# Kernel optimization log

Hardware: AMD Instinct MI355X
Metric: run time of the kernel (lower is better)

The kernel has to match this reference:

```python
import jax, jax.numpy as jnp
import numpy as np

SHIFT_CONSTRAINT = 1000.0
TWO_PI = 2.0 * np.pi


def setup_inputs() -> dict:
    key = jax.random.key(0)
    k1, k2, k3, k4 = jax.random.split(key, 4)
    N, M, rank = 1000, 4000, 8
    X = jax.random.normal(k1, (N, M), dtype=jnp.float32)
    C_tilde = jax.random.uniform(k2, (rank, N), dtype=jnp.float32)
    S_tilde = jax.random.uniform(k3, (N, rank), dtype=jnp.float32)
    tau_tilde = jax.random.normal(k4, (N, rank), dtype=jnp.float32)
    return {"X": X, "C_tilde": C_tilde, "S_tilde": S_tilde, "tau_tilde": tau_tilde}


def reference(X, C_tilde, S_tilde, tau_tilde):
    N, M = X.shape
    f = jnp.arange(M, dtype=X.dtype) / M                      # [M]
    tau = jnp.tanh(tau_tilde) * SHIFT_CONSTRAINT              # [N, d]
    # phase argument: 2*pi*tau[N,d]*f[M] -> [N, d, M]
    arg = TWO_PI * jnp.einsum('Nd,M->NdM', tau, f)
    omega = jnp.exp(-1j * arg)                                # exp(-i 2pi tau f)
    omega_neg = jnp.conj(omega)                               # exp(+i 2pi tau f)
    C = jax.nn.softmax(C_tilde, axis=0)                       # [d, N]
    S = jax.nn.softmax(S_tilde, axis=1)                       # [N, d]
    X_F = jnp.fft.fft(X)                                      # [N, M] complex
    X_align = X_F[:, None, :] * omega_neg                     # [N, d, M]
    A = jnp.einsum('dN,NdM->dM', C.astype(omega.dtype), X_align)
    A_shift = A[None, :, :] * omega                           # [N, d, M]
    recon = jnp.einsum('Nd,NdM->NM', S.astype(omega.dtype), A_shift)
    # residual in frequency-domain-reconstruction space (complex, as in torch)
    return X.astype(recon.dtype) - recon
```

## Files before the change

kernel.cpp:

```cpp
#include <hip/hip_runtime.h>
#include <math.h>

#define N_ROWS 1000
#define M_COLS 4000
#define RANK 8
#define M1 50
#define M2 80
#define NCHUNK 40
#define CHUNK 25
#define TWO_PI_F 6.28318530717958647692f

__device__ float  g_tau[N_ROWS * RANK];
__device__ float2 g_stp[N_ROWS * RANK];
__device__ float  g_Cw [RANK * N_ROWS];
__device__ float  g_Sw [N_ROWS * RANK];
__device__ float2 g_XF [N_ROWS * M_COLS];
__device__ float2 g_P  [NCHUNK * RANK * M_COLS];
__device__ float2 g_A  [RANK * M_COLS];

__device__ __forceinline__ unsigned short bf16_rne(float f) {
    unsigned int u = __float_as_uint(f);
    return (unsigned short)((u + 0x7FFFu + ((u >> 16) & 1u)) >> 16);
}

__device__ __forceinline__ void fast_sincos(float tau, float fm, float* sn, float* cs) {
    float p = tau * fm;
    float r = p - floorf(p);
    float ang = TWO_PI_F * r;
    *sn = __sinf(ang);
    *cs = __cosf(ang);
}

__device__ __forceinline__ void compute_params_row(int n,
                                                   const float* __restrict__ Ct,
                                                   const float* __restrict__ St,
                                                   const float* __restrict__ Tt) {
    #pragma unroll
    for (int d = 0; d < RANK; ++d) {
        float t = tanhf(Tt[n*RANK + d]) * 1000.0f;
        g_tau[n*RANK + d] = t;
        float sn, cs;
        float p = t * (1.0f / (float)M_COLS);
        p = p - floorf(p);
        sincosf(TWO_PI_F * p, &sn, &cs);
        g_stp[n*RANK + d] = make_float2(cs, sn);
    }

    float v[RANK];
    float mx = -1e30f;
    #pragma unroll
    for (int d = 0; d < RANK; ++d) { v[d] = Ct[d*N_ROWS + n]; mx = fmaxf(mx, v[d]); }
    float s = 0.f;
    #pragma unroll
    for (int d = 0; d < RANK; ++d) { v[d] = expf(v[d] - mx); s += v[d]; }
    float inv = 1.f / s;
    #pragma unroll
    for (int d = 0; d < RANK; ++d) g_Cw[d*N_ROWS + n] = v[d] * inv;

    mx = -1e30f;
    #pragma unroll
    for (int d = 0; d < RANK; ++d) { v[d] = St[n*RANK + d]; mx = fmaxf(mx, v[d]); }
    s = 0.f;
    #pragma unroll
    for (int d = 0; d < RANK; ++d) { v[d] = expf(v[d] - mx); s += v[d]; }
    inv = 1.f / s;
    #pragma unroll
    for (int d = 0; d < RANK; ++d) g_Sw[n*RANK + d] = v[d] * inv;
}

__global__ __launch_bounds__(512) void k_fft(const float* __restrict__ X,
                                             const float* __restrict__ Ct,
                                             const float* __restrict__ St,
                                             const float* __restrict__ Tt) {
    __shared__ float2 lX2[M_COLS];
    __shared__ float2 lY0[M1 * 21];
    __shared__ float2 lY1[M1 * 21];

    const int half = blockIdx.x;
    if (blockIdx.y == 500) {
        if (half == 0)
            for (int n = threadIdx.x; n < N_ROWS; n += 512)
                compute_params_row(n, Ct, St, Tt);
        return;
    }

    const int r0 = blockIdx.y * 2, r1 = r0 + 1;
    const int m2base = half ? 21 : 0;
    const int HM2    = half ? 20 : 21;
    const float* __restrict__ x0 = X + r0 * M_COLS;
    const float* __restrict__ x1 = X + r1 * M_COLS;

    for (int j = threadIdx.x; j < M_COLS; j += 512)
        lX2[j] = make_float2(x0[j], x1[j]);
    __syncthreads();

    for (int t = threadIdx.x; t < M1 * HM2; t += 512) {
        int k1 = t / HM2;
        int m2 = m2base + (t - k1 * HM2);
        float sn, cs;
        sincosf((TWO_PI_F / (float)M2) * (float)m2, &sn, &cs);
        float sr = cs, si = -sn;
        float wr = 1.f, wi = 0.f;
        float a0r = 0.f, a0i = 0.f, a1r = 0.f, a1i = 0.f;
        #pragma unroll 4
        for (int k2 = 0; k2 < M2; ++k2) {
            float2 xv = lX2[k1 + M1 * k2];
            a0r = fmaf(xv.x, wr, a0r);
            a0i = fmaf(xv.x, wi, a0i);
            a1r = fmaf(xv.y, wr, a1r);
            a1i = fmaf(xv.y, wi, a1i);
            float nr = fmaf(wr, sr, -wi * si);
            float ni = fmaf(wr, si,  wi * sr);
            wr = nr; wi = ni;
        }
        lY0[t] = make_float2(a0r, a0i);
        lY1[t] = make_float2(a1r, a1i);
    }
    __syncthreads();

    float2* __restrict__ XF0 = g_XF + r0 * M_COLS;
    float2* __restrict__ XF1 = g_XF + r1 * M_COLS;
    const int tot = half ? 975 : 1026;
    for (int t = threadIdx.x; t < tot; t += 512) {
        int m1, m2;
        if (half == 0) {
            if (t < 1000) { m1 = t / 20; m2 = 1 + (t - m1 * 20); }
            else          { m1 = t - 1000; m2 = 0; }
        } else {
            if (t < 950)  { m1 = t / 19; m2 = 21 + (t - m1 * 19); }
            else          { m1 = t - 950; m2 = 40; }
        }
        int m = m1 * M2 + m2;
        float sn, cs;
        sincosf((TWO_PI_F / (float)M_COLS) * (float)m, &sn, &cs);
        float sr = cs, si = -sn;
        float wr = 1.f, wi = 0.f;
        float a0r = 0.f, a0i = 0.f, a1r = 0.f, a1i = 0.f;
        int m2l = m2 - m2base;
        #pragma unroll 5
        for (int k1 = 0; k1 < M1; ++k1) {
            float2 y0 = lY0[k1 * HM2 + m2l];
            float2 y1 = lY1[k1 * HM2 + m2l];
            a0r = fmaf(y0.x, wr, fmaf(-y0.y, wi, a0r));
            a0i = fmaf(y0.x, wi, fmaf( y0.y, wr, a0i));
            a1r = fmaf(y1.x, wr, fmaf(-y1.y, wi, a1r));
            a1i = fmaf(y1.x, wi, fmaf( y1.y, wr, a1i));
            float nr = fmaf(wr, sr, -wi * si);
            float ni = fmaf(wr, si,  wi * sr);
            wr = nr; wi = ni;
        }
        XF0[m] = make_float2(a0r, a0i);
        XF1[m] = make_float2(a1r, a1i);
        if (m != 0 && m != 2000) {
            XF0[M_COLS - m] = make_float2(a0r, -a0i);
            XF1[M_COLS - m] = make_float2(a1r, -a1i);
        }
    }
}

__global__ __launch_bounds__(256) void k_accA() {
    int m = blockIdx.x * 256 + threadIdx.x;
    int chunk = blockIdx.y;
    if (m >= M_COLS) return;
    float fm = (float)m / 4000.0f;

    float accr[RANK], acci[RANK];
    #pragma unroll
    for (int d = 0; d < RANK; ++d) { accr[d] = 0.f; acci[d] = 0.f; }

    int n0 = chunk * CHUNK;
    for (int n = n0; n < n0 + CHUNK; ++n) {
        float2 xf = g_XF[n * M_COLS + m];
        #pragma unroll
        for (int d = 0; d < RANK; ++d) {
            float tau = g_tau[n*RANK + d];
            float cv  = g_Cw[d*N_ROWS + n];
            float sn, cs;
            fast_sincos(tau, fm, &sn, &cs);
            accr[d] = fmaf(cv, xf.x * cs - xf.y * sn, accr[d]);
            acci[d] = fmaf(cv, xf.x * sn + xf.y * cs, acci[d]);
        }
    }
    #pragma unroll
    for (int d = 0; d < RANK; ++d)
        g_P[(chunk*RANK + d)*M_COLS + m] = make_float2(accr[d], acci[d]);
}

__global__ __launch_bounds__(256) void k_reduceA() {
    int i = blockIdx.x * 256 + threadIdx.x;
    int d = i / M_COLS;
    int m = i - d * M_COLS;
    float ar = 0.f, ai = 0.f;
    for (int c = 0; c < NCHUNK; ++c) {
        float2 p = g_P[(c*RANK + d)*M_COLS + m];
        ar += p.x; ai += p.y;
    }
    g_A[i] = make_float2(ar, ai);
}

__global__ __launch_bounds__(256) void k_recon(const float* __restrict__ X,
                                               unsigned short* __restrict__ out16) {
    int strip = blockIdx.x * 256 + threadIdx.x;
    int m0 = strip * 4;
    int n = blockIdx.y;
    if (m0 >= M_COLS) return;
    float fm0 = (float)m0 / 4000.0f;

    float outr[4], outi[4];
    #pragma unroll
    for (int j = 0; j < 4; ++j) {
        outr[j] = X[n*M_COLS + m0 + j];
        outi[j] = 0.f;
    }
    #pragma unroll
    for (int d = 0; d < RANK; ++d) {
        float tau = g_tau[n*RANK + d];
        float sv  = g_Sw[n*RANK + d];
        float2 st = g_stp[n*RANK + d];
        float sn, cs;
        fast_sincos(tau, fm0, &sn, &cs);
        float wr = cs, wi = -sn;
        float str =  st.x, sti = -st.y;
        #pragma unroll
        for (int j = 0; j < 4; ++j) {
            float2 a = g_A[d*M_COLS + m0 + j];
            outr[j] -= sv * fmaf(a.x, wr, -a.y * wi);
            outi[j] -= sv * fmaf(a.x, wi,  a.y * wr);
            float nr = fmaf(wr, str, -wi * sti);
            float ni = fmaf(wr, sti,  wi * str);
            wr = nr; wi = ni;
        }
    }
    long e0 = (long)n * M_COLS + m0;
    unsigned short r[4], iM[4];
    #pragma unroll
    for (int j = 0; j < 4; ++j) { r[j] = bf16_rne(outr[j]); iM[j] = bf16_rne(outi[j]); }
    out16[2*e0 + 1] = r[0];
    unsigned int* w32 = (unsigned int*)(out16 + 2*e0 + 2);
    w32[0] = (unsigned int)iM[0] | ((unsigned int)r[1] << 16);
    w32[1] = (unsigned int)iM[1] | ((unsigned int)r[2] << 16);
    w32[2] = (unsigned int)iM[2] | ((unsigned int)r[3] << 16);
    out16[2*e0 + 8] = iM[3];
}

extern "C" void kernel_launch(void* const* d_in, const int* in_sizes, int n_in,
                              void* d_out, int out_size, void* d_ws, size_t ws_size,
                              hipStream_t stream) {
    const float* X  = nullptr;
    const float* sm[3] = {nullptr, nullptr, nullptr};
    int nsm = 0;
    for (int i = 0; i < n_in; ++i) {
        if (in_sizes[i] == N_ROWS * M_COLS) X = (const float*)d_in[i];
        else if (nsm < 3)                   sm[nsm++] = (const float*)d_in[i];
    }
    const float* Ct = sm[0];
    const float* St = sm[1];
    const float* Tt = sm[2];
    (void)d_ws; (void)ws_size;

    k_fft    <<<dim3(2, 501),     dim3(512), 0, stream>>>(X, Ct, St, Tt);
    k_accA   <<<dim3(16, NCHUNK), dim3(256), 0, stream>>>();
    k_reduceA<<<dim3(125),        dim3(256), 0, stream>>>();
    k_recon  <<<dim3(4, N_ROWS),  dim3(256), 0, stream>>>(X, (unsigned short*)d_out);
}
```

Baseline: 85.24 us.

## Replace two-stage 50x80 DFT with multi-stage mixed-radix FFT per row

The row FFT moves from a two-stage 50x80 direct DFT, which processed two rows per block split across two halves, to a deeper mixed-radix factorization: radix-10, radix-8, radix-5 and radix-10 passes with shared-memory twiddle tables. Each block now handles one row, and Hermitian symmetry is used in the middle stages and on output. The aim is to cut the O(M*(M1+M2)) FLOP count of the DFT stage. In exchange there are more synchronisation barriers and more shared-memory traffic, and the two-row reuse per load is lost.

Result: faster. 77.16 us, median of 3 (-9.5%).

```diff
diff --git a/kernel.cpp b/kernel.cpp
--- a/kernel.cpp
+++ b/kernel.cpp
@@ -4,8 +4,6 @@
 #define N_ROWS 1000
 #define M_COLS 4000
 #define RANK 8
-#define M1 50
-#define M2 80
 #define NCHUNK 40
 #define CHUNK 25
 #define TWO_PI_F 6.28318530717958647692f
@@ -72,89 +70,111 @@
                                              const float* __restrict__ Ct,
                                              const float* __restrict__ St,
                                              const float* __restrict__ Tt) {
-    __shared__ float2 lX2[M_COLS];
-    __shared__ float2 lY0[M1 * 21];
-    __shared__ float2 lY1[M1 * 21];
-
-    const int half = blockIdx.x;
-    if (blockIdx.y == 500) {
-        if (half == 0)
-            for (int n = threadIdx.x; n < N_ROWS; n += 512)
-                compute_params_row(n, Ct, St, Tt);
+    __shared__ float2 R1[4000];
+    __shared__ float2 R2[2050];
+    __shared__ float2 T10[10];
+    __shared__ float2 T80[80];
+    __shared__ float2 T400[400];
+
+    if (blockIdx.x == 1000) {
+        for (int n = threadIdx.x; n < N_ROWS; n += 512)
+            compute_params_row(n, Ct, St, Tt);
         return;
     }
 
-    const int r0 = blockIdx.y * 2, r1 = r0 + 1;
-    const int m2base = half ? 21 : 0;
-    const int HM2    = half ? 20 : 21;
-    const float* __restrict__ x0 = X + r0 * M_COLS;
-    const float* __restrict__ x1 = X + r1 * M_COLS;
+    const int row = blockIdx.x;
+    const float* __restrict__ x = X + row * M_COLS;
+    float* lX = (float*)R2;
 
     for (int j = threadIdx.x; j < M_COLS; j += 512)
-        lX2[j] = make_float2(x0[j], x1[j]);
-    __syncthreads();
-
-    for (int t = threadIdx.x; t < M1 * HM2; t += 512) {
-        int k1 = t / HM2;
-        int m2 = m2base + (t - k1 * HM2);
-        float sn, cs;
-        sincosf((TWO_PI_F / (float)M2) * (float)m2, &sn, &cs);
-        float sr = cs, si = -sn;
-        float wr = 1.f, wi = 0.f;
-        float a0r = 0.f, a0i = 0.f, a1r = 0.f, a1i = 0.f;
-        #pragma unroll 4
-        for (int k2 = 0; k2 < M2; ++k2) {
-            float2 xv = lX2[k1 + M1 * k2];
-            a0r = fmaf(xv.x, wr, a0r);
-            a0i = fmaf(xv.x, wi, a0i);
-            a1r = fmaf(xv.y, wr, a1r);
-            a1i = fmaf(xv.y, wi, a1i);
-            float nr = fmaf(wr, sr, -wi * si);
-            float ni = fmaf(wr, si,  wi * sr);
-            wr = nr; wi = ni;
-        }
-        lY0[t] = make_float2(a0r, a0i);
-        lY1[t] = make_float2(a1r, a1i);
-    }
-    __syncthreads();
-
-    float2* __restrict__ XF0 = g_XF + r0 * M_COLS;
-    float2* __restrict__ XF1 = g_XF + r1 * M_COLS;
-    const int tot = half ? 975 : 1026;
-    for (int t = threadIdx.x; t < tot; t += 512) {
+        lX[j] = x[j];
+    for (int j = threadIdx.x; j < 490; j += 512) {
+        int jj; float ang; float2* dst;
+        if (j < 10)      { jj = j;      ang = (TWO_PI_F / 10.0f)  * (float)jj; dst = &T10[jj]; }
+        else if (j < 90) { jj = j - 10; ang = (TWO_PI_F / 80.0f)  * (float)jj; dst = &T80[jj]; }
+        else             { jj = j - 90; ang = (TWO_PI_F / 400.0f) * (float)jj; dst = &T400[jj]; }
+        float sn, cs; sincosf(ang, &sn, &cs);
+        *dst = make_float2(cs, -sn);
+    }
+    __syncthreads();
+
+    for (int t = threadIdx.x; t < 4000; t += 512) {
+        int k1 = t / 80; int rr = t - k1 * 80; int r8 = rr / 10; int u = rr - r8 * 10;
+        int xb = k1 + 50 * r8;
+        float ar = 0.f, ai = 0.f; int idx = 0;
+        #pragma unroll
+        for (int s = 0; s < 10; ++s) {
+            float xv = lX[xb + 400 * s];
+            float2 w = T10[idx];
+            ar = fmaf(xv, w.x, ar);
+            ai = fmaf(xv, w.y, ai);
+            idx += u; if (idx >= 10) idx -= 10;
+        }
+        R1[t] = make_float2(ar, ai);
+    }
+    __syncthreads();
+
+    for (int t = threadIdx.x; t < 2050; t += 512) {
+        int k1 = t / 41; int m2 = t - k1 * 41; int u = m2 % 10;
+        int zb = k1 * 80 + u;
+        float ar = 0.f, ai = 0.f; int idx = 0;
+        #pragma unroll
+        for (int r = 0; r < 8; ++r) {
+            float2 z = R1[zb + 10 * r];
+            float2 w = T80[idx];
+            ar = fmaf(z.x, w.x, fmaf(-z.y, w.y, ar));
+            ai = fmaf(z.x, w.y, fmaf( z.y, w.x, ai));
+            idx += m2; if (idx >= 80) idx -= 80;
+        }
+        R2[t] = make_float2(ar, ai);
+    }
+    __syncthreads();
+
+    for (int t = threadIdx.x; t < 4000; t += 512) {
+        int r10 = t / 400; int q = t - r10 * 400;
+        int m2q = q % 80;
+        int yi; float sgn;
+        if (m2q <= 40) { yi = m2q;      sgn =  1.f; }
+        else           { yi = 80 - m2q; sgn = -1.f; }
+        float ar = 0.f, ai = 0.f; int idx = 0;
+        #pragma unroll
+        for (int s = 0; s < 5; ++s) {
+            float2 y = R2[(r10 + 10 * s) * 41 + yi];
+            float yy = sgn * y.y;
+            float2 w = T400[idx];
+            ar = fmaf(y.x, w.x, fmaf(-yy, w.y, ar));
+            ai = fmaf(y.x, w.y, fmaf( yy, w.x, ai));
+            idx += q; if (idx >= 400) idx -= 400;
+        }
+        R1[t] = make_float2(ar, ai);
+    }
+    __syncthreads();
+
+    float2* __restrict__ XFr = g_XF + row * M_COLS;
+    for (int t = threadIdx.x; t < 2001; t += 512) {
         int m1, m2;
-        if (half == 0) {
-            if (t < 1000) { m1 = t / 20; m2 = 1 + (t - m1 * 20); }
-            else          { m1 = t - 1000; m2 = 0; }
-        } else {
-            if (t < 950)  { m1 = t / 19; m2 = 21 + (t - m1 * 19); }
-            else          { m1 = t - 950; m2 = 40; }
-        }
-        int m = m1 * M2 + m2;
+        if (t < 1950)      { m1 = t / 39; m2 = 1 + (t - m1 * 39); }
+        else if (t < 1976) { m1 = t - 1950; m2 = 0; }
+        else               { m1 = t - 1976; m2 = 40; }
+        int m = m1 * 80 + m2;
+        int q = m % 400;
         float sn, cs;
         sincosf((TWO_PI_F / (float)M_COLS) * (float)m, &sn, &cs);
         float sr = cs, si = -sn;
         float wr = 1.f, wi = 0.f;
-        float a0r = 0.f, a0i = 0.f, a1r = 0.f, a1i = 0.f;
-        int m2l = m2 - m2base;
-        #pragma unroll 5
-        for (int k1 = 0; k1 < M1; ++k1) {
-            float2 y0 = lY0[k1 * HM2 + m2l];
-            float2 y1 = lY1[k1 * HM2 + m2l];
-            a0r = fmaf(y0.x, wr, fmaf(-y0.y, wi, a0r));
-            a0i = fmaf(y0.x, wi, fmaf( y0.y, wr, a0i));
-            a1r = fmaf(y1.x, wr, fmaf(-y1.y, wi, a1r));
-            a1i = fmaf(y1.x, wi, fmaf( y1.y, wr, a1i));
+        float ar = 0.f, ai = 0.f;
+        #pragma unroll
+        for (int r = 0; r < 10; ++r) {
+            float2 b = R1[r * 400 + q];
+            ar = fmaf(b.x, wr, fmaf(-b.y, wi, ar));
+            ai = fmaf(b.x, wi, fmaf( b.y, wr, ai));
             float nr = fmaf(wr, sr, -wi * si);
             float ni = fmaf(wr, si,  wi * sr);
             wr = nr; wi = ni;
         }
-        XF0[m] = make_float2(a0r, a0i);
-        XF1[m] = make_float2(a1r, a1i);
-        if (m != 0 && m != 2000) {
-            XF0[M_COLS - m] = make_float2(a0r, -a0i);
-            XF1[M_COLS - m] = make_float2(a1r, -a1i);
-        }
+        XFr[m] = make_float2(ar, ai);
+        if (m != 0 && m != 2000)
+            XFr[M_COLS - m] = make_float2(ar, -ai);
     }
 }
 
@@ -258,7 +278,7 @@
     const float* Tt = sm[2];
     (void)d_ws; (void)ws_size;
 
-    k_fft    <<<dim3(2, 501),     dim3(512), 0, stream>>>(X, Ct, St, Tt);
+    k_fft    <<<dim3(1001),       dim3(512), 0, stream>>>(X, Ct, St, Tt);
     k_accA   <<<dim3(16, NCHUNK), dim3(256), 0, stream>>>();
     k_reduceA<<<dim3(125),        dim3(256), 0, stream>>>();
     k_recon  <<<dim3(4, N_ROWS),  dim3(256), 0, stream>>>(X, (unsigned short*)d_out);
```
